# Kernel tuning notes

Hardware: AMD Instinct MI355X
Metric: run time of the kernel (lower is better)

## Reference

```python
import jax, jax.numpy as jnp
import numpy as np

INPUTDIM = 256
OUTDIM = 256
GRIDSIZE = 300
SCALE_BASE = 1.0
SCALE_FOURIER = 1.0
BATCH = 2048


def setup_inputs() -> dict:
    key = jax.random.key(0)
    k_x, k_bw, k_fc = jax.random.split(key, 3)
    x = jax.random.normal(k_x, (BATCH, INPUTDIM), dtype=jnp.float32)
    # HeUniform for base_weight: limit = sqrt(6 / fan_in)
    limit = np.sqrt(6.0 / INPUTDIM)
    base_weight = jax.random.uniform(
        k_bw, (INPUTDIM, OUTDIM), dtype=jnp.float32, minval=-limit, maxval=limit)
    stddev = 1.0 / (np.sqrt(INPUTDIM) * np.sqrt(GRIDSIZE))
    fouriercoeffs = (jax.random.normal(k_fc, (2, OUTDIM, INPUTDIM, GRIDSIZE), dtype=jnp.float32)
                     * jnp.float32(stddev))
    return {"x": x, "base_weight": base_weight, "fouriercoeffs": fouriercoeffs}


def reference(x, base_weight, fouriercoeffs):
    # Base path: silu(x @ W)
    base_output = jax.nn.silu(x @ base_weight)  # [B, J]
    # Fourier feature expansion: k = 1..gridsize
    k = jnp.arange(1, GRIDSIZE + 1, dtype=x.dtype)  # [K]
    theta = x[:, :, None] * k[None, None, :]        # [B, I, K]
    c = jnp.cos(theta)
    s = jnp.sin(theta)
    # einsum 'dbik,djik->bj' split into cos and sin parts
    fourier_output = (jnp.einsum('bik,jik->bj', c, fouriercoeffs[0])
                      + jnp.einsum('bik,jik->bj', s, fouriercoeffs[1]))
    return SCALE_BASE * base_output + SCALE_FOURIER * fourier_output
```

## Files before the change

### kernel.cpp

```cpp
#include <hip/hip_runtime.h>
#include <hip/hip_bf16.h>
#include <cstdint>

#define BATCH   2048
#define INDIM   256
#define OUTDIM  256
#define KGRID   300
#define NCHUNK  10

typedef __attribute__((ext_vector_type(4))) float f32x4;
typedef __attribute__((ext_vector_type(2))) float f32x2;
typedef __attribute__((ext_vector_type(8))) short bf16x8;

__device__ __forceinline__ uint32_t pack_bf16x2(float lo, float hi) {
    union { __hip_bfloat162 h; uint32_t u; } cv;
    cv.h = __float22bfloat162_rn(make_float2(lo, hi));
    return cv.u;
}

__device__ __forceinline__ f32x2 pk_fma_sub(f32x2 a, f32x2 b, f32x2 c) {
    f32x2 d;
    asm("v_pk_fma_f32 %0, %1, %2, %3 neg_lo:[0,0,1] neg_hi:[0,0,1]"
        : "=v"(d) : "v"(a), "v"(b), "v"(c));
    return d;
}

__device__ __forceinline__ void load_lds16(const void* g, void* l) {
    __builtin_amdgcn_global_load_lds(
        (const __attribute__((address_space(1))) void*)g,
        (__attribute__((address_space(3))) void*)l, 16, 0, 0);
}

__device__ __forceinline__ bf16x8 zero_frag() {
    union { uint32_t u[4]; bf16x8 v; } z = {{0u, 0u, 0u, 0u}};
    return z.v;
}

__device__ __forceinline__ bf16x8 gen_frag(float ck, float sk,
                                           float c1, float s1) {
    float cp = __builtin_fmaf(ck, c1,  sk * s1);
    float sp = __builtin_fmaf(sk, c1, -ck * s1);
    f32x2 C; C.x = ck; C.y = sk;
    f32x2 P; P.x = cp; P.y = sp;
    f32x2 T2; T2.x = c1 + c1; T2.y = c1 + c1;
    union { uint32_t u[4]; bf16x8 v; } r;
    #pragma unroll
    for (int q = 0; q < 4; ++q) {
        r.u[q] = pack_bf16x2(C.x, C.y);
        f32x2 N = pk_fma_sub(T2, C, P);
        P = C; C = N;
    }
    return r.v;
}

#define PACKED_U4 ((size_t)INDIM * NCHUNK * OUTDIM * 8)
#define PACKED_BYTES (PACKED_U4 * 16)

__global__ __launch_bounds__(256) void pack_kernel(
    const float* __restrict__ fc, uint4* __restrict__ pk)
{
    size_t tidg = (size_t)blockIdx.x * 256 + threadIdx.x;
    int sub = tidg & 7;
    int j   = (tidg >> 3) & 255;
    int ich = (int)(tidg >> 11);
    int ch  = ich % NCHUNK;
    int i   = ich / NCHUNK;
    int kb  = ch * 32 + (sub ^ (j & 7)) * 4;
    if (kb > KGRID - 4) kb = KGRID - 4;
    const float* pc = fc + ((size_t)j * INDIM + i) * KGRID + kb;
    const float* ps = pc + (size_t)OUTDIM * INDIM * KGRID;
    float4 vc = *reinterpret_cast<const float4*>(pc);
    float4 vs = *reinterpret_cast<const float4*>(ps);
    uint4 wv;
    wv.x = pack_bf16x2(vc.x, vs.x);
    wv.y = pack_bf16x2(vc.y, vs.y);
    wv.z = pack_bf16x2(vc.z, vs.z);
    wv.w = pack_bf16x2(vc.w, vs.w);
    pk[tidg] = wv;
}

__global__ __launch_bounds__(256, 2) void fourier_dma_kernel(
    const float* __restrict__ x, const uint4* __restrict__ pk,
    float* __restrict__ part)
{
    __shared__ uint4 Bbuf[2][256][8];

    const int tid = threadIdx.x;
    const int flat = blockIdx.x + (blockIdx.z << 4);
    const int L  = (flat & 7) * 64 + (flat >> 3);
    const int b0 = (L & 15) * 128;
    const int z  = L >> 4;
    const int i0 = z * 8;

    const int lane = tid & 63, wave = tid >> 6;
    const int wrow = wave * 32;
    const int lrow = lane & 15, lgrp = lane >> 4;
    const int q8 = wave * 8;

    f32x4 acc[2][16] = {};

    float thn[2];
    float c1[2], s1[2];
    float c16[2], s16[2];
    float cS[2], sS[2];

    #pragma unroll
    for (int mf = 0; mf < 2; ++mf)
        thn[mf] = x[(size_t)(b0 + wrow + mf * 16 + lrow) * INDIM + i0];

    {
        const uint4* src = pk + (size_t)(i0 * NCHUNK) * 2048;
        char* dst = (char*)&Bbuf[0][0][0];
        #pragma unroll
        for (int q = 0; q < 8; ++q)
            load_lds16(src + (q8 + q) * 64 + lane, dst + (q8 + q) * 1024);
    }

    int il = 0, ch = 0;
    #pragma unroll 1
    for (int t = 0; t < 8 * NCHUNK; ++t) {
        {
            int il2 = il, ch2 = ch + 1;
            if (ch2 == NCHUNK) { ch2 = 0; il2 = (il + 1 < 8) ? il + 1 : il; }
            const uint4* src = pk + (size_t)((i0 + il2) * NCHUNK + ch2) * 2048;
            char* dst = (char*)&Bbuf[(t + 1) & 1][0][0];
            #pragma unroll
            for (int q = 0; q < 8; ++q)
                load_lds16(src + (q8 + q) * 64 + lane, dst + (q8 + q) * 1024);
        }
        if (ch == 0) {
            const float flg = (float)(lgrp * 4);
            #pragma unroll
            for (int mf = 0; mf < 2; ++mf) {
                float th = thn[mf];
                __sincosf(th, &s1[mf], &c1[mf]);
                __sincosf(16.f * th, &s16[mf], &c16[mf]);
                float a0 = __builtin_fmaf(flg, th, th);
                __sincosf(a0, &sS[mf], &cS[mf]);
            }
            int iln = (il + 1 < 8) ? il + 1 : il;
            #pragma unroll
            for (int mf = 0; mf < 2; ++mf)
                thn[mf] = x[(size_t)(b0 + wrow + mf * 16 + lrow) * INDIM
                            + i0 + iln];
        }
        bf16x8 af[2][2];
        #pragma unroll
        for (int mf = 0; mf < 2; ++mf) {
            af[0][mf] = gen_frag(cS[mf], sS[mf], c1[mf], s1[mf]);
            float ck = __builtin_fmaf(cS[mf], c16[mf], -sS[mf] * s16[mf]);
            float sk = __builtin_fmaf(sS[mf], c16[mf],  cS[mf] * s16[mf]);
            af[1][mf] = gen_frag(ck, sk, c1[mf], s1[mf]);
            cS[mf] = __builtin_fmaf(ck, c16[mf], -sk * s16[mf]);
            sS[mf] = __builtin_fmaf(sk, c16[mf],  ck * s16[mf]);
        }
        if (ch == NCHUNK - 1) {
            #pragma unroll
            for (int mf = 0; mf < 2; ++mf) {
                af[0][mf] = (lgrp == 3) ? zero_frag() : af[0][mf];
                af[1][mf] = zero_frag();
            }
        }
        __syncthreads();
        __builtin_amdgcn_s_setprio(1);
        #pragma unroll
        for (int s = 0; s < 2; ++s) {
            const int swz = (s * 4 + lgrp) ^ (lrow & 7);
            #pragma unroll
            for (int g = 0; g < 4; ++g) {
                bf16x8 bfr[4];
                #pragma unroll
                for (int q = 0; q < 4; ++q) {
                    const int jl = (g * 4 + q) * 16 + lrow;
                    uint4 tv = Bbuf[t & 1][jl][swz];
                    bfr[q] = *reinterpret_cast<bf16x8*>(&tv);
                }
                #pragma unroll
                for (int mf = 0; mf < 2; ++mf)
                    #pragma unroll
                    for (int q = 0; q < 4; ++q)
                        acc[mf][g * 4 + q] = __builtin_amdgcn_mfma_f32_16x16x32_bf16(
                            af[s][mf], bfr[q], acc[mf][g * 4 + q], 0, 0, 0);
            }
        }
        __builtin_amdgcn_s_setprio(0);
        __syncthreads();
        if (++ch == NCHUNK) { ch = 0; ++il; }
    }

    float* pws = part + (size_t)z * BATCH * OUTDIM;
    #pragma unroll
    for (int mf = 0; mf < 2; ++mf)
        #pragma unroll
        for (int nf = 0; nf < 16; ++nf)
            #pragma unroll
            for (int r = 0; r < 4; ++r) {
                int b = b0 + wrow + mf * 16 + lgrp * 4 + r;
                int j = nf * 16 + lrow;
                pws[(size_t)b * OUTDIM + j] = acc[mf][nf][r];
            }
}

__global__ __launch_bounds__(256, 2) void fourier_kernel_fb(
    const float* __restrict__ x, const float* __restrict__ fc,
    float* __restrict__ ws, int ips)
{
    __shared__ uint4 Abuf[2][128][8];
    __shared__ uint4 Bbuf[128][8];

    const int tid  = threadIdx.x;
    const int b0   = blockIdx.x * 256;
    const int j0   = blockIdx.y * 128;
    const int i0   = blockIdx.z * ips;

    const int lane = tid & 63, wave = tid >> 6;
    const int wm   = wave >> 1, wn = wave & 1;
    const int lrow = lane & 15, lgrp = lane >> 4;
    const int grow = tid >> 1,  gh = tid & 1;

    f32x4 acc[2][4][4] = {};

    #pragma unroll 1
    for (int il = 0; il < ips; ++il) {
        const int i = i0 + il;
        float th[2], c1[2], s1[2], t2[2];
        th[0] = x[(size_t)(b0 + grow)       * INDIM + i];
        th[1] = x[(size_t)(b0 + 128 + grow) * INDIM + i];
        #pragma unroll
        for (int m = 0; m < 2; ++m) {
            __sincosf(th[m], &s1[m], &c1[m]);
            t2[m] = 2.f * c1[m];
        }
        #pragma unroll 1
        for (int ch = 0; ch < NCHUNK; ++ch) {
            #pragma unroll
            for (int r = 0; r < 4; ++r) {
                int flat = r * 256 + tid;
                int jl = flat >> 3, sub = flat & 7;
                int kb = ch * 32 + sub * 4;
                if (kb > KGRID - 4) kb = KGRID - 4;
                const float* pc = fc + ((size_t)(j0 + jl) * INDIM + i) * KGRID + kb;
                const float* ps = pc + (size_t)OUTDIM * INDIM * KGRID;
                float4 vc = *reinterpret_cast<const float4*>(pc);
                float4 vs = *reinterpret_cast<const float4*>(ps);
                uint4 wv;
                wv.x = pack_bf16x2(vc.x, vs.x);
                wv.y = pack_bf16x2(vc.y, vs.y);
                wv.z = pack_bf16x2(vc.z, vs.z);
                wv.w = pack_bf16x2(vc.w, vs.w);
                Bbuf[jl][sub ^ (jl & 7)] = wv;
            }
            #pragma unroll
            for (int m = 0; m < 2; ++m) {
                const int k0 = ch * 32 + gh * 16;
                float ck, sk;
                __sincosf(th[m] * (float)(k0 + 1), &sk, &ck);
                float cp = __builtin_fmaf(ck, c1[m],  sk * s1[m]);
                float sp = __builtin_fmaf(sk, c1[m], -ck * s1[m]);
                const int swz = grow & 7;
                #pragma unroll
                for (int c = 0; c < 4; ++c) {
                    uint32_t uu[4];
                    #pragma unroll
                    for (int qq = 0; qq < 4; ++qq) {
                        const int kidx = k0 + c * 4 + qq;
                        float cc = (kidx < KGRID) ? ck : 0.f;
                        float ss = (kidx < KGRID) ? sk : 0.f;
                        uu[qq] = pack_bf16x2(cc, ss);
                        float cn = __builtin_fmaf(t2[m], ck, -cp);
                        float sn = __builtin_fmaf(t2[m], sk, -sp);
                        cp = ck; sp = sk; ck = cn; sk = sn;
                    }
                    Abuf[m][grow][(gh * 4 + c) ^ swz] =
                        make_uint4(uu[0], uu[1], uu[2], uu[3]);
                }
            }
            __syncthreads();
            #pragma unroll
            for (int s = 0; s < 2; ++s) {
                bf16x8 bfr[4];
                #pragma unroll
                for (int nf = 0; nf < 4; ++nf) {
                    const int jl = wn * 64 + nf * 16 + lrow;
                    uint4 tv = Bbuf[jl][(s * 4 + lgrp) ^ (jl & 7)];
                    bfr[nf] = *reinterpret_cast<bf16x8*>(&tv);
                }
                #pragma unroll
                for (int m = 0; m < 2; ++m) {
                    #pragma unroll
                    for (int mf = 0; mf < 4; ++mf) {
                        const int rowA = wm * 64 + mf * 16 + lrow;
                        uint4 tv = Abuf[m][rowA][(s * 4 + lgrp) ^ (rowA & 7)];
                        bf16x8 af = *reinterpret_cast<bf16x8*>(&tv);
                        #pragma unroll
                        for (int nf = 0; nf < 4; ++nf)
                            acc[m][mf][nf] = __builtin_amdgcn_mfma_f32_16x16x32_bf16(
                                af, bfr[nf], acc[m][mf][nf], 0, 0, 0);
                    }
                }
            }
            __syncthreads();
        }
    }

    float* pws = ws + (size_t)blockIdx.z * BATCH * OUTDIM;
    #pragma unroll
    for (int m = 0; m < 2; ++m)
        #pragma unroll
        for (int mf = 0; mf < 4; ++mf)
            #pragma unroll
            for (int nf = 0; nf < 4; ++nf)
                #pragma unroll
                for (int r = 0; r < 4; ++r) {
                    int b = b0 + m * 128 + wm * 64 + mf * 16 + lgrp * 4 + r;
                    int j = j0 + wn * 64 + nf * 16 + lrow;
                    pws[(size_t)b * OUTDIM + j] = acc[m][mf][nf][r];
                }
}

__global__ __launch_bounds__(256) void combine_kernel(
    const float* __restrict__ x, const float* __restrict__ w,
    const float* __restrict__ part, float* __restrict__ out, int nsplit)
{
    __shared__ float Xs[64][16];
    __shared__ float Wt[16][68];

    const int tid = threadIdx.x;
    const int b0 = blockIdx.x * 64;
    const int j0 = blockIdx.y * 64;
    const int tx = tid & 15, ty = tid >> 4;

    float acc[4][4] = {};

    for (int kb = 0; kb < INDIM; kb += 16) {
        {
            int m = tid >> 2, kq = (tid & 3) * 4;
            float4 v = *reinterpret_cast<const float4*>(
                &x[(size_t)(b0 + m) * INDIM + kb + kq]);
            Xs[m][kq+0] = v.x; Xs[m][kq+1] = v.y; Xs[m][kq+2] = v.z; Xs[m][kq+3] = v.w;
        }
        {
            int kr = tid >> 4, jc = (tid & 15) * 4;
            float4 v = *reinterpret_cast<const float4*>(
                &w[(size_t)(kb + kr) * OUTDIM + j0 + jc]);
            Wt[kr][jc+0] = v.x; Wt[kr][jc+1] = v.y; Wt[kr][jc+2] = v.z; Wt[kr][jc+3] = v.w;
        }
        __syncthreads();
        #pragma unroll
        for (int kk = 0; kk < 16; ++kk) {
            float a[4], b[4];
            #pragma unroll
            for (int q = 0; q < 4; ++q) { a[q] = Xs[ty*4+q][kk]; b[q] = Wt[kk][tx*4+q]; }
            #pragma unroll
            for (int q = 0; q < 4; ++q)
                #pragma unroll
                for (int p = 0; p < 4; ++p)
                    acc[q][p] = __builtin_fmaf(a[q], b[p], acc[q][p]);
        }
        __syncthreads();
    }

    float psum[4][4] = {};
    for (int s = 0; s < nsplit; ++s) {
        const float* base = part + (size_t)s * BATCH * OUTDIM;
        #pragma unroll
        for (int q = 0; q < 4; ++q) {
            float4 pv = *reinterpret_cast<const float4*>(
                &base[(size_t)(b0 + ty*4 + q) * OUTDIM + j0 + tx*4]);
            psum[q][0] += pv.x; psum[q][1] += pv.y;
            psum[q][2] += pv.z; psum[q][3] += pv.w;
        }
    }

    #pragma unroll
    for (int q = 0; q < 4; ++q)
        #pragma unroll
        for (int p = 0; p < 4; ++p) {
            float v = acc[q][p];
            float sv = v / (1.f + __expf(-v));
            out[(size_t)(b0 + ty*4 + q) * OUTDIM + (j0 + tx*4 + p)] =
                sv + psum[q][p];
        }
}

extern "C" void kernel_launch(void* const* d_in, const int* in_sizes, int n_in,
                              void* d_out, int out_size, void* d_ws, size_t ws_size,
                              hipStream_t stream) {
    const float* x  = (const float*)d_in[0];
    const float* bw = (const float*)d_in[1];
    const float* fc = (const float*)d_in[2];
    float* out = (float*)d_out;

    const size_t per = (size_t)BATCH * OUTDIM * sizeof(float);

    if (ws_size >= PACKED_BYTES + 32 * per) {
        uint4* pk   = (uint4*)d_ws;
        float* part = (float*)((char*)d_ws + PACKED_BYTES);
        pack_kernel<<<(int)(PACKED_U4 / 256), 256, 0, stream>>>(fc, pk);
        fourier_dma_kernel<<<dim3(16, 1, 32), 256, 0, stream>>>(x, pk, part);
        combine_kernel<<<dim3(BATCH / 64, OUTDIM / 64), 256, 0, stream>>>(
            x, bw, part, out, 32);
    } else {
        float* part = (float*)d_ws;
        int S = 32;
        while (S > 1 && (size_t)S * per > ws_size) S >>= 1;
        const int ips = INDIM / S;
        fourier_kernel_fb<<<dim3(BATCH / 256, OUTDIM / 128, S), 256, 0, stream>>>(
            x, fc, part, ips);
        combine_kernel<<<dim3(BATCH / 64, OUTDIM / 64), 256, 0, stream>>>(
            x, bw, part, out, S);
    }
}
```

Before: 223.6 us.

## Switch Fourier DMA kernel to 32x32x16 bf16 MFMA tiles

Replaces the 16x16x32 MFMA inner loop with 32x32x16 MFMAs, so each wave covers its 32 batch rows with one A fragment per k-step instead of two. The per-lane trig recurrence is reorganised to one row per lane, stepping by 8 harmonics across four k-substeps, and the LDS read indexing, tail-chunk zero masking and output store mapping are rewritten to match the 32x32 accumulator layout. The aim is fewer MFMA issues and fewer A-fragment generations per LDS B read. In exchange the per-lane sin/cos work is serialised inside the MFMA loop, and the changed LDS access pattern could cause bank conflicts.

Measured after the change: 247.7 us. 10.8% more time.

```diff
diff --git a/kernel.cpp b/kernel.cpp
--- a/kernel.cpp
+++ b/kernel.cpp
@@ -8,9 +8,10 @@
 #define KGRID   300
 #define NCHUNK  10
 
-typedef __attribute__((ext_vector_type(4))) float f32x4;
-typedef __attribute__((ext_vector_type(2))) float f32x2;
-typedef __attribute__((ext_vector_type(8))) short bf16x8;
+typedef __attribute__((ext_vector_type(4)))  float f32x4;
+typedef __attribute__((ext_vector_type(16))) float f32x16;
+typedef __attribute__((ext_vector_type(2)))  float f32x2;
+typedef __attribute__((ext_vector_type(8)))  short bf16x8;
 
 __device__ __forceinline__ uint32_t pack_bf16x2(float lo, float hi) {
     union { __hip_bfloat162 h; uint32_t u; } cv;
@@ -92,21 +93,20 @@
     const int z  = L >> 4;
     const int i0 = z * 8;
 
-    const int lane = tid & 63, wave = tid >> 6;
-    const int wrow = wave * 32;
-    const int lrow = lane & 15, lgrp = lane >> 4;
+    const int lane  = tid & 63, wave = tid >> 6;
+    const int wrow  = wave * 32;
+    const int col   = lane & 31;
+    const int khalf = lane >> 5;
     const int q8 = wave * 8;
 
-    f32x4 acc[2][16] = {};
-
-    float thn[2];
-    float c1[2], s1[2];
-    float c16[2], s16[2];
-    float cS[2], sS[2];
-
-    #pragma unroll
-    for (int mf = 0; mf < 2; ++mf)
-        thn[mf] = x[(size_t)(b0 + wrow + mf * 16 + lrow) * INDIM + i0];
+    f32x16 acc[8] = {};
+
+    float thn;
+    float c1v, s1v;
+    float c8v, s8v;
+    float cSv, sSv;
+
+    thn = x[(size_t)(b0 + wrow + col) * INDIM + i0];
 
     {
         const uint4* src = pk + (size_t)(i0 * NCHUNK) * 2048;
@@ -129,58 +129,51 @@
                 load_lds16(src + (q8 + q) * 64 + lane, dst + (q8 + q) * 1024);
         }
         if (ch == 0) {
-            const float flg = (float)(lgrp * 4);
-            #pragma unroll
-            for (int mf = 0; mf < 2; ++mf) {
-                float th = thn[mf];
-                __sincosf(th, &s1[mf], &c1[mf]);
-                __sincosf(16.f * th, &s16[mf], &c16[mf]);
-                float a0 = __builtin_fmaf(flg, th, th);
-                __sincosf(a0, &sS[mf], &cS[mf]);
-            }
+            float th = thn;
+            __sincosf(th, &s1v, &c1v);
+            __sincosf(8.f * th, &s8v, &c8v);
+            float a0 = __builtin_fmaf((float)(khalf * 4), th, th);
+            __sincosf(a0, &sSv, &cSv);
             int iln = (il + 1 < 8) ? il + 1 : il;
-            #pragma unroll
-            for (int mf = 0; mf < 2; ++mf)
-                thn[mf] = x[(size_t)(b0 + wrow + mf * 16 + lrow) * INDIM
-                            + i0 + iln];
-        }
-        bf16x8 af[2][2];
-        #pragma unroll
-        for (int mf = 0; mf < 2; ++mf) {
-            af[0][mf] = gen_frag(cS[mf], sS[mf], c1[mf], s1[mf]);
-            float ck = __builtin_fmaf(cS[mf], c16[mf], -sS[mf] * s16[mf]);
-            float sk = __builtin_fmaf(sS[mf], c16[mf],  cS[mf] * s16[mf]);
-            af[1][mf] = gen_frag(ck, sk, c1[mf], s1[mf]);
-            cS[mf] = __builtin_fmaf(ck, c16[mf], -sk * s16[mf]);
-            sS[mf] = __builtin_fmaf(sk, c16[mf],  ck * s16[mf]);
-        }
-        if (ch == NCHUNK - 1) {
-            #pragma unroll
-            for (int mf = 0; mf < 2; ++mf) {
-                af[0][mf] = (lgrp == 3) ? zero_frag() : af[0][mf];
-                af[1][mf] = zero_frag();
-            }
+            thn = x[(size_t)(b0 + wrow + col) * INDIM + i0 + iln];
+        }
+        bf16x8 af0 = gen_frag(cSv, sSv, c1v, s1v);
+        {
+            float cn = __builtin_fmaf(cSv, c8v, -sSv * s8v);
+            float sn = __builtin_fmaf(sSv, c8v,  cSv * s8v);
+            cSv = cn; sSv = sn;
         }
         __syncthreads();
         __builtin_amdgcn_s_setprio(1);
         #pragma unroll
-        for (int s = 0; s < 2; ++s) {
-            const int swz = (s * 4 + lgrp) ^ (lrow & 7);
-            #pragma unroll
-            for (int g = 0; g < 4; ++g) {
+        for (int ks = 0; ks < 4; ++ks) {
+            bf16x8 af;
+            if (ks == 0) {
+                af = af0;
+            } else {
+                af = gen_frag(cSv, sSv, c1v, s1v);
+                float cn = __builtin_fmaf(cSv, c8v, -sSv * s8v);
+                float sn = __builtin_fmaf(sSv, c8v,  cSv * s8v);
+                cSv = cn; sSv = sn;
+                if (ch == NCHUNK - 1) {
+                    if (ks >= 2) af = zero_frag();
+                    else if (khalf) af = zero_frag();
+                }
+            }
+            const int swzb = ks * 2 + khalf;
+            #pragma unroll
+            for (int g = 0; g < 2; ++g) {
                 bf16x8 bfr[4];
                 #pragma unroll
                 for (int q = 0; q < 4; ++q) {
-                    const int jl = (g * 4 + q) * 16 + lrow;
-                    uint4 tv = Bbuf[t & 1][jl][swz];
+                    const int jl = (g * 4 + q) * 32 + col;
+                    uint4 tv = Bbuf[t & 1][jl][swzb ^ (jl & 7)];
                     bfr[q] = *reinterpret_cast<bf16x8*>(&tv);
                 }
                 #pragma unroll
-                for (int mf = 0; mf < 2; ++mf)
-                    #pragma unroll
-                    for (int q = 0; q < 4; ++q)
-                        acc[mf][g * 4 + q] = __builtin_amdgcn_mfma_f32_16x16x32_bf16(
-                            af[s][mf], bfr[q], acc[mf][g * 4 + q], 0, 0, 0);
+                for (int q = 0; q < 4; ++q)
+                    acc[g * 4 + q] = __builtin_amdgcn_mfma_f32_32x32x16_bf16(
+                        af, bfr[q], acc[g * 4 + q], 0, 0, 0);
             }
         }
         __builtin_amdgcn_s_setprio(0);
@@ -190,15 +183,13 @@
 
     float* pws = part + (size_t)z * BATCH * OUTDIM;
     #pragma unroll
-    for (int mf = 0; mf < 2; ++mf)
-        #pragma unroll
-        for (int nf = 0; nf < 16; ++nf)
-            #pragma unroll
-            for (int r = 0; r < 4; ++r) {
-                int b = b0 + wrow + mf * 16 + lgrp * 4 + r;
-                int j = nf * 16 + lrow;
-                pws[(size_t)b * OUTDIM + j] = acc[mf][nf][r];
-            }
+    for (int jt = 0; jt < 8; ++jt)
+        #pragma unroll
+        for (int r = 0; r < 16; ++r) {
+            int b = b0 + wrow + (r & 3) + 8 * (r >> 2) + 4 * khalf;
+            int j = jt * 32 + col;
+            pws[(size_t)b * OUTDIM + j] = acc[jt][r];
+        }
 }
 
 __global__ __launch_bounds__(256, 2) void fourier_kernel_fb(
```
